# Optimization experiments

Measured on AMD Instinct MI355X. Metric: run time of the kernel, lower is better.

## Reference

```python
import jax, jax.numpy as jnp
import numpy as np

B, T, F_IN, F_OUT = 16, 2048, 128, 128
ALPHA = 0.2  # LeakyReLU negative slope
MASK_VAL = -1e9


def setup_inputs() -> dict:
    key = jax.random.key(0)
    kx, kw, ka, kadj = jax.random.split(key, 4)
    # xavier_uniform-ish scale for W and a (gain=1.414)
    w_bound = 1.414 * np.sqrt(6.0 / (F_IN + F_OUT))
    a_bound = 1.414 * np.sqrt(6.0 / (2 * F_OUT + 1))
    x = jax.random.normal(kx, (B, T, F_IN), jnp.float32)
    W = jax.random.uniform(kw, (F_IN, F_OUT), jnp.float32, -w_bound, w_bound)
    a = jax.random.uniform(ka, (2 * F_OUT, 1), jnp.float32, -a_bound, a_bound)
    adj = jax.random.randint(kadj, (B, T, T), 0, 2, jnp.int32)
    return {"x": x, "adj": adj, "W": W, "a": a}


def reference(x, adj, W, a):
    # h: [B,T,F_OUT]
    h = jnp.einsum('btf,fo->bto', x, W)
    # Additive GAT score decomposition: e[b,i,j] = leakyrelu(h_i . a1 + h_j . a2)
    # Mathematically identical to cat([h_i,h_j]) @ a, without the BxTxTx2F tensor.
    a1 = a[:F_OUT, 0]   # [F_OUT]
    a2 = a[F_OUT:, 0]   # [F_OUT]
    s1 = h @ a1         # [B,T]
    s2 = h @ a2         # [B,T]
    e = jax.nn.leaky_relu(s1[:, :, None] + s2[:, None, :], ALPHA)  # [B,T,T]
    e = jnp.where(adj == 0, MASK_VAL, e)
    att = jax.nn.softmax(e, axis=-1)  # [B,T,T]
    # dropout=0.0 / eval mode -> identity
    return att @ h  # [B,T,F_OUT]
```

## Files before the change

kernel.cpp:

```cpp
#include <hip/hip_runtime.h>

#define TT 2048
#define NB 16
#define FD 128
#define ALPHA 0.2f

typedef __attribute__((ext_vector_type(8))) short short8;
typedef __attribute__((ext_vector_type(4))) float f32x4;
typedef __attribute__((ext_vector_type(16))) float f32x16;

static __device__ __forceinline__ unsigned short f2bf(float f) {
    unsigned u = __float_as_uint(f);
    u += 0x7FFF + ((u >> 16) & 1);
    return (unsigned short)(u >> 16);
}
static __device__ __forceinline__ float bf2f(unsigned short s) {
    return __uint_as_float(((unsigned)s) << 16);
}

__global__ __launch_bounds__(256) void k_pack(const int* __restrict__ adj,
                                              unsigned char* __restrict__ bm)
{
    const int tid = threadIdx.x;
    const int w = tid >> 6, l = tid & 63;
    const int row = blockIdx.x * 4 + w;
    const int* ap = adj + (size_t)row * TT;
    unsigned char* op = bm + (size_t)row * 256;

    #pragma unroll
    for (int rd = 0; rd < 8; ++rd) {
        int4 q = *reinterpret_cast<const int4*>(ap + rd * 256 + l * 4);
        unsigned long long m0 = __ballot(q.x != 0);
        unsigned long long m1 = __ballot(q.y != 0);
        unsigned long long m2 = __ballot(q.z != 0);
        unsigned long long m3 = __ballot(q.w != 0);
        if (l < 32) {
            unsigned b =
                 ((unsigned)(m0 >> (2 * l)) & 1)
              | (((unsigned)(m1 >> (2 * l)) & 1) << 1)
              | (((unsigned)(m2 >> (2 * l)) & 1) << 2)
              | (((unsigned)(m3 >> (2 * l)) & 1) << 3)
              | (((unsigned)(m0 >> (2 * l + 1)) & 1) << 4)
              | (((unsigned)(m1 >> (2 * l + 1)) & 1) << 5)
              | (((unsigned)(m2 >> (2 * l + 1)) & 1) << 6)
              | (((unsigned)(m3 >> (2 * l + 1)) & 1) << 7);
            op[rd * 32 + l] = (unsigned char)b;
        }
    }
}

__global__ __launch_bounds__(256) void k_wt(const float* __restrict__ W,
                                            unsigned short* __restrict__ WT)
{
    int fid = blockIdx.x * 256 + threadIdx.x;
    int k = fid >> 5;
    int f = (fid & 31) << 2;
    float4 w4 = *reinterpret_cast<const float4*>(W + k * FD + f);
    WT[(f + 0) * FD + k] = f2bf(w4.x);
    WT[(f + 1) * FD + k] = f2bf(w4.y);
    WT[(f + 2) * FD + k] = f2bf(w4.z);
    WT[(f + 3) * FD + k] = f2bf(w4.w);
}

__global__ __launch_bounds__(256) void k_h(const float* __restrict__ x,
                                           const unsigned short* __restrict__ WT,
                                           const float* __restrict__ a,
                                           unsigned short* __restrict__ hF,
                                           float* __restrict__ s1,
                                           float* __restrict__ s2)
{
    __shared__ unsigned short hs[128][72];

    const int tid = threadIdx.x;
    const int b  = blockIdx.x >> 5;
    const int t0 = (blockIdx.x & 31) << 6;
    const int w = tid >> 6, l = tid & 63, g = l >> 4, r15 = l & 15;

    const float* xrow = x + ((size_t)(b * TT + t0 + w * 16 + r15)) * FD;

    f32x4 acc[8] = {};

    #pragma unroll
    for (int m = 0; m < 4; ++m) {
        const int koff = m * 32 + g * 8;
        float4 xa = *reinterpret_cast<const float4*>(xrow + koff);
        float4 xb = *reinterpret_cast<const float4*>(xrow + koff + 4);
        short8 af;
        af[0] = (short)f2bf(xa.x); af[1] = (short)f2bf(xa.y);
        af[2] = (short)f2bf(xa.z); af[3] = (short)f2bf(xa.w);
        af[4] = (short)f2bf(xb.x); af[5] = (short)f2bf(xb.y);
        af[6] = (short)f2bf(xb.z); af[7] = (short)f2bf(xb.w);
        #pragma unroll
        for (int n = 0; n < 8; ++n) {
            short8 bfr = *reinterpret_cast<const short8*>(WT + (n * 16 + r15) * FD + koff);
            acc[n] = __builtin_amdgcn_mfma_f32_16x16x32_bf16(af, bfr, acc[n], 0, 0, 0);
        }
    }

    float p1[4] = {0.f, 0.f, 0.f, 0.f}, p2[4] = {0.f, 0.f, 0.f, 0.f};
    #pragma unroll
    for (int n = 0; n < 8; ++n) {
        float a1v = a[n * 16 + r15];
        float a2v = a[FD + n * 16 + r15];
        #pragma unroll
        for (int r = 0; r < 4; ++r) {
            p1[r] += acc[n][r] * a1v;
            p2[r] += acc[n][r] * a2v;
        }
    }
    #pragma unroll
    for (int r = 0; r < 4; ++r) {
        #pragma unroll
        for (int off = 8; off >= 1; off >>= 1) {
            p1[r] += __shfl_xor(p1[r], off);
            p2[r] += __shfl_xor(p2[r], off);
        }
    }
    if (r15 == 0) {
        const int trow = t0 + w * 16 + g * 4;
        #pragma unroll
        for (int r = 0; r < 4; ++r) {
            s1[b * TT + trow + r] = p1[r];
            s2[b * TT + trow + r] = p2[r];
        }
    }

    #pragma unroll
    for (int n = 0; n < 8; ++n)
        #pragma unroll
        for (int r = 0; r < 4; ++r)
            hs[n * 16 + r15][w * 16 + g * 4 + r] = f2bf(acc[n][r]);
    __syncthreads();

    #pragma unroll
    for (int it = 0; it < 4; ++it) {
        int idx = it * 256 + tid;
        int lp = idx & 63;
        int frag = idx >> 6;
        int n32 = frag & 3, tl = frag >> 2;
        int fsrc = n32 * 32 + (lp & 31);
        int tsrc = tl * 16 + (lp >> 5) * 8;
        short8 v = *reinterpret_cast<const short8*>(&hs[fsrc][tsrc]);
        *reinterpret_cast<short8*>(
            hF + (((size_t)(b * 128 + (t0 >> 4) + tl)) * 4 + n32) * 512 + lp * 8) = v;
    }
}

__global__ __launch_bounds__(256, 4) void k_att(const unsigned char* __restrict__ bm,
                                                const unsigned short* __restrict__ hF,
                                                const float* __restrict__ s1,
                                                const float* __restrict__ s2,
                                                float* __restrict__ out)
{
    __shared__ __align__(16) float red[2][32][132];
    __shared__ float dsum[4][32];

    const int tid = threadIdx.x;
    const int wg = (blockIdx.x & 7) * 128 + (blockIdx.x >> 3);
    const int b  = wg >> 6;
    const int i0 = (wg & 63) << 5;
    const int w = tid >> 6, l = tid & 63;
    const int il = l & 31, h = l >> 5;
    const int hsh = h * 8;

    const int jbeg = w * (TT / 4);
    const float s1v = s1[b * TT + i0 + il];
    const float* s2p = s2 + b * TT + jbeg + h * 8;
    const unsigned char* bmrow = bm + ((size_t)(b * TT + i0 + il)) * 256 + w * 64;
    const unsigned short* hfp = hF + ((size_t)(b * 128 + (jbeg >> 4))) * 4 * 512 + l * 8;

    f32x16 acc[4] = {};
    float rsum = 0.f;

    short8 bb[2][4];
    #pragma unroll
    for (int n = 0; n < 4; ++n)
        bb[0][n] = *reinterpret_cast<const short8*>(hfp + (size_t)n * 512);

    uint4 bq;

    #pragma unroll
    for (int t = 0; t < 32; ++t) {
        const int cur = t & 1;
        if (t < 31) {
            #pragma unroll
            for (int n = 0; n < 4; ++n)
                bb[cur ^ 1][n] = *reinterpret_cast<const short8*>(
                    hfp + (size_t)((t + 1) * 4 + n) * 512);
        }
        if ((t & 7) == 0)
            bq = *reinterpret_cast<const uint4*>(bmrow + (t >> 3) * 16);
        const int wi = (t & 7) >> 1;
        const unsigned wsel = wi == 0 ? bq.x : wi == 1 ? bq.y : wi == 2 ? bq.z : bq.w;
        const unsigned bits = (wsel >> ((t & 1) * 16 + hsh)) & 0xffu;

        float4 sa = *reinterpret_cast<const float4*>(s2p + t * 16);
        float4 sb = *reinterpret_cast<const float4*>(s2p + t * 16 + 4);
        float csf[8] = {sa.x, sa.y, sa.z, sa.w, sb.x, sb.y, sb.z, sb.w};
        short8 af;
        #pragma unroll
        for (int e = 0; e < 8; ++e) {
            float s = s1v + csf[e];
            s = fmaxf(s, ALPHA * s);
            float p = ((bits >> e) & 1) ? __expf(s) : 0.f;
            unsigned short u = f2bf(p);
            rsum += bf2f(u);
            af[e] = (short)u;
        }
        #pragma unroll
        for (int n = 0; n < 4; ++n)
            acc[n] = __builtin_amdgcn_mfma_f32_32x32x16_bf16(af, bb[cur][n], acc[n], 0, 0, 0);
    }

    rsum += __shfl_xor(rsum, 32);
    if (l < 32) dsum[w][l] = rsum;

    if (w < 2) {
        #pragma unroll
        for (int n = 0; n < 4; ++n)
            #pragma unroll
            for (int r = 0; r < 16; ++r) {
                int irow = (r & 3) + 8 * (r >> 2) + 4 * h;
                red[w][irow][n * 32 + il] = acc[n][r];
            }
    }
    __syncthreads();
    if (w >= 2) {
        #pragma unroll
        for (int n = 0; n < 4; ++n)
            #pragma unroll
            for (int r = 0; r < 16; ++r) {
                int irow = (r & 3) + 8 * (r >> 2) + 4 * h;
                red[w - 2][irow][n * 32 + il] += acc[n][r];
            }
    }
    __syncthreads();

    #pragma unroll
    for (int it = 0; it < 4; ++it) {
        int e = it * 256 + tid;
        int row = e >> 5;
        int c4 = (e & 31) << 2;
        float4 v0 = *reinterpret_cast<const float4*>(&red[0][row][c4]);
        float4 v1 = *reinterpret_cast<const float4*>(&red[1][row][c4]);
        float dn = dsum[0][row] + dsum[1][row] + dsum[2][row] + dsum[3][row];
        float ri = 1.0f / dn;
        float4 o;
        o.x = (v0.x + v1.x) * ri;
        o.y = (v0.y + v1.y) * ri;
        o.z = (v0.z + v1.z) * ri;
        o.w = (v0.w + v1.w) * ri;
        *reinterpret_cast<float4*>(out + ((size_t)(b * TT + i0 + row)) * FD + c4) = o;
    }
}

extern "C" void kernel_launch(void* const* d_in, const int* in_sizes, int n_in,
                              void* d_out, int out_size, void* d_ws, size_t ws_size,
                              hipStream_t stream)
{
    const float* x  = (const float*)d_in[0];
    const int* adj  = (const int*)d_in[1];
    const float* W  = (const float*)d_in[2];
    const float* a  = (const float*)d_in[3];
    float* out = (float*)d_out;

    unsigned short* hF = (unsigned short*)d_ws;
    float* s1 = (float*)((char*)d_ws + (size_t)NB * FD * TT * 2);
    float* s2 = s1 + NB * TT;
    unsigned short* WT = (unsigned short*)(s2 + NB * TT);
    unsigned char* bm = (unsigned char*)(WT + FD * FD);

    k_pack<<<NB * TT / 4, 256, 0, stream>>>(adj, bm);
    k_wt  <<<16, 256, 0, stream>>>(W, WT);
    k_h   <<<NB * (TT / 64), 256, 0, stream>>>(x, WT, a, hF, s1, s2);
    k_att <<<NB * (TT / 32), 256, 0, stream>>>(bm, hF, s1, s2, out);
}
```

Baseline: 103.7 us.

## Merge adjacency packing, W transpose and h projection into one prep kernel

Replaces three prologue kernels with a single k_prep launch. The first 512 blocks each transpose and convert W into LDS themselves and compute h, s1 and s2. The remaining blocks pack the adjacency into a bitmask. This removes two kernel launches and their serialization, and lets the bandwidth-heavy adj packing overlap with the projection. In exchange, every projection block redundantly rebuilds the bf16 W^T in shared memory, and the larger LDS footprint may lower occupancy for the packing blocks.

After: 106.2 us. 2.5% more time.

```diff
diff --git a/kernel.cpp b/kernel.cpp
--- a/kernel.cpp
+++ b/kernel.cpp
@@ -18,63 +18,63 @@
     return __uint_as_float(((unsigned)s) << 16);
 }
 
-__global__ __launch_bounds__(256) void k_pack(const int* __restrict__ adj,
+__global__ __launch_bounds__(256) void k_prep(const float* __restrict__ x,
+                                              const float* __restrict__ W,
+                                              const float* __restrict__ a,
+                                              const int* __restrict__ adj,
+                                              unsigned short* __restrict__ hF,
+                                              float* __restrict__ s1,
+                                              float* __restrict__ s2,
                                               unsigned char* __restrict__ bm)
 {
+    __shared__ unsigned short lds[128 * 136];
+
     const int tid = threadIdx.x;
     const int w = tid >> 6, l = tid & 63;
-    const int row = blockIdx.x * 4 + w;
-    const int* ap = adj + (size_t)row * TT;
-    unsigned char* op = bm + (size_t)row * 256;
-
-    #pragma unroll
-    for (int rd = 0; rd < 8; ++rd) {
-        int4 q = *reinterpret_cast<const int4*>(ap + rd * 256 + l * 4);
-        unsigned long long m0 = __ballot(q.x != 0);
-        unsigned long long m1 = __ballot(q.y != 0);
-        unsigned long long m2 = __ballot(q.z != 0);
-        unsigned long long m3 = __ballot(q.w != 0);
-        if (l < 32) {
-            unsigned b =
-                 ((unsigned)(m0 >> (2 * l)) & 1)
-              | (((unsigned)(m1 >> (2 * l)) & 1) << 1)
-              | (((unsigned)(m2 >> (2 * l)) & 1) << 2)
-              | (((unsigned)(m3 >> (2 * l)) & 1) << 3)
-              | (((unsigned)(m0 >> (2 * l + 1)) & 1) << 4)
-              | (((unsigned)(m1 >> (2 * l + 1)) & 1) << 5)
-              | (((unsigned)(m2 >> (2 * l + 1)) & 1) << 6)
-              | (((unsigned)(m3 >> (2 * l + 1)) & 1) << 7);
-            op[rd * 32 + l] = (unsigned char)b;
-        }
-    }
-}
-
-__global__ __launch_bounds__(256) void k_wt(const float* __restrict__ W,
-                                            unsigned short* __restrict__ WT)
-{
-    int fid = blockIdx.x * 256 + threadIdx.x;
-    int k = fid >> 5;
-    int f = (fid & 31) << 2;
-    float4 w4 = *reinterpret_cast<const float4*>(W + k * FD + f);
-    WT[(f + 0) * FD + k] = f2bf(w4.x);
-    WT[(f + 1) * FD + k] = f2bf(w4.y);
-    WT[(f + 2) * FD + k] = f2bf(w4.z);
-    WT[(f + 3) * FD + k] = f2bf(w4.w);
-}
-
-__global__ __launch_bounds__(256) void k_h(const float* __restrict__ x,
-                                           const unsigned short* __restrict__ WT,
-                                           const float* __restrict__ a,
-                                           unsigned short* __restrict__ hF,
-                                           float* __restrict__ s1,
-                                           float* __restrict__ s2)
-{
-    __shared__ unsigned short hs[128][72];
-
-    const int tid = threadIdx.x;
+
+    if (blockIdx.x >= 512) {
+        const int row = (blockIdx.x - 512) * 4 + w;
+        const int* ap = adj + (size_t)row * TT;
+        unsigned char* op = bm + (size_t)row * 256;
+
+        #pragma unroll
+        for (int rd = 0; rd < 8; ++rd) {
+            int4 q = *reinterpret_cast<const int4*>(ap + rd * 256 + l * 4);
+            unsigned long long m0 = __ballot(q.x != 0);
+            unsigned long long m1 = __ballot(q.y != 0);
+            unsigned long long m2 = __ballot(q.z != 0);
+            unsigned long long m3 = __ballot(q.w != 0);
+            if (l < 32) {
+                unsigned b =
+                     ((unsigned)(m0 >> (2 * l)) & 1)
+                  | (((unsigned)(m1 >> (2 * l)) & 1) << 1)
+                  | (((unsigned)(m2 >> (2 * l)) & 1) << 2)
+                  | (((unsigned)(m3 >> (2 * l)) & 1) << 3)
+                  | (((unsigned)(m0 >> (2 * l + 1)) & 1) << 4)
+                  | (((unsigned)(m1 >> (2 * l + 1)) & 1) << 5)
+                  | (((unsigned)(m2 >> (2 * l + 1)) & 1) << 6)
+                  | (((unsigned)(m3 >> (2 * l + 1)) & 1) << 7);
+                op[rd * 32 + l] = (unsigned char)b;
+            }
+        }
+        return;
+    }
+
     const int b  = blockIdx.x >> 5;
     const int t0 = (blockIdx.x & 31) << 6;
-    const int w = tid >> 6, l = tid & 63, g = l >> 4, r15 = l & 15;
+    const int g = l >> 4, r15 = l & 15;
+
+    for (int it = 0; it < 16; ++it) {
+        int fid = it * 256 + tid;
+        int k = fid >> 5;
+        int f = (fid & 31) << 2;
+        float4 w4 = *reinterpret_cast<const float4*>(W + k * FD + f);
+        lds[(f + 0) * 136 + k] = f2bf(w4.x);
+        lds[(f + 1) * 136 + k] = f2bf(w4.y);
+        lds[(f + 2) * 136 + k] = f2bf(w4.z);
+        lds[(f + 3) * 136 + k] = f2bf(w4.w);
+    }
+    __syncthreads();
 
     const float* xrow = x + ((size_t)(b * TT + t0 + w * 16 + r15)) * FD;
 
@@ -92,7 +92,7 @@
         af[6] = (short)f2bf(xb.z); af[7] = (short)f2bf(xb.w);
         #pragma unroll
         for (int n = 0; n < 8; ++n) {
-            short8 bfr = *reinterpret_cast<const short8*>(WT + (n * 16 + r15) * FD + koff);
+            short8 bfr = *reinterpret_cast<const short8*>(&lds[(n * 16 + r15) * 136 + koff]);
             acc[n] = __builtin_amdgcn_mfma_f32_16x16x32_bf16(af, bfr, acc[n], 0, 0, 0);
         }
     }
@@ -125,11 +125,13 @@
         }
     }
 
+    __syncthreads();
+
     #pragma unroll
     for (int n = 0; n < 8; ++n)
         #pragma unroll
         for (int r = 0; r < 4; ++r)
-            hs[n * 16 + r15][w * 16 + g * 4 + r] = f2bf(acc[n][r]);
+            lds[(n * 16 + r15) * 72 + w * 16 + g * 4 + r] = f2bf(acc[n][r]);
     __syncthreads();
 
     #pragma unroll
@@ -140,7 +142,7 @@
         int n32 = frag & 3, tl = frag >> 2;
         int fsrc = n32 * 32 + (lp & 31);
         int tsrc = tl * 16 + (lp >> 5) * 8;
-        short8 v = *reinterpret_cast<const short8*>(&hs[fsrc][tsrc]);
+        short8 v = *reinterpret_cast<const short8*>(&lds[fsrc * 72 + tsrc]);
         *reinterpret_cast<short8*>(
             hF + (((size_t)(b * 128 + (t0 >> 4) + tl)) * 4 + n32) * 512 + lp * 8) = v;
     }
@@ -267,11 +269,8 @@
     unsigned short* hF = (unsigned short*)d_ws;
     float* s1 = (float*)((char*)d_ws + (size_t)NB * FD * TT * 2);
     float* s2 = s1 + NB * TT;
-    unsigned short* WT = (unsigned short*)(s2 + NB * TT);
-    unsigned char* bm = (unsigned char*)(WT + FD * FD);
-
-    k_pack<<<NB * TT / 4, 256, 0, stream>>>(adj, bm);
-    k_wt  <<<16, 256, 0, stream>>>(W, WT);
-    k_h   <<<NB * (TT / 64), 256, 0, stream>>>(x, WT, a, hF, s1, s2);
+    unsigned char* bm = (unsigned char*)(s2 + NB * TT);
+
+    k_prep<<<512 + NB * TT / 4, 256, 0, stream>>>(x, W, a, adj, hF, s1, s2, bm);
     k_att <<<NB * (TT / 32), 256, 0, stream>>>(bm, hF, s1, s2, out);
 }
```

## Merge adjacency packing into h projection kernel and use intrinsic bf16 conversion

Applied to the files above, without the earlier changes.

Folds the adjacency bit-packing kernel into the h/score projection kernel: the first 512 blocks compute h and the scores, and the remaining blocks pack the mask. This removes one launch and lets the two independent prep stages run at the same time. The attention inner loop now sums the row denominator from fp32 probabilities instead of the bf16-rounded values, tests mask bits with a shift and sign check, and converts to bf16 through the HIP intrinsic. The denominator now differs slightly from the bf16 numerator weights, and launch_bounds(256,8) may limit registers in the merged kernel.

Result: no change. 104.6 us (+0.9%).

```diff
diff --git a/kernel.cpp b/kernel.cpp
--- a/kernel.cpp
+++ b/kernel.cpp
@@ -1,4 +1,5 @@
 #include <hip/hip_runtime.h>
+#include <hip/hip_bf16.h>
 
 #define TT 2048
 #define NB 16
@@ -14,39 +15,8 @@
     u += 0x7FFF + ((u >> 16) & 1);
     return (unsigned short)(u >> 16);
 }
-static __device__ __forceinline__ float bf2f(unsigned short s) {
-    return __uint_as_float(((unsigned)s) << 16);
-}
-
-__global__ __launch_bounds__(256) void k_pack(const int* __restrict__ adj,
-                                              unsigned char* __restrict__ bm)
-{
-    const int tid = threadIdx.x;
-    const int w = tid >> 6, l = tid & 63;
-    const int row = blockIdx.x * 4 + w;
-    const int* ap = adj + (size_t)row * TT;
-    unsigned char* op = bm + (size_t)row * 256;
-
-    #pragma unroll
-    for (int rd = 0; rd < 8; ++rd) {
-        int4 q = *reinterpret_cast<const int4*>(ap + rd * 256 + l * 4);
-        unsigned long long m0 = __ballot(q.x != 0);
-        unsigned long long m1 = __ballot(q.y != 0);
-        unsigned long long m2 = __ballot(q.z != 0);
-        unsigned long long m3 = __ballot(q.w != 0);
-        if (l < 32) {
-            unsigned b =
-                 ((unsigned)(m0 >> (2 * l)) & 1)
-              | (((unsigned)(m1 >> (2 * l)) & 1) << 1)
-              | (((unsigned)(m2 >> (2 * l)) & 1) << 2)
-              | (((unsigned)(m3 >> (2 * l)) & 1) << 3)
-              | (((unsigned)(m0 >> (2 * l + 1)) & 1) << 4)
-              | (((unsigned)(m1 >> (2 * l + 1)) & 1) << 5)
-              | (((unsigned)(m2 >> (2 * l + 1)) & 1) << 6)
-              | (((unsigned)(m3 >> (2 * l + 1)) & 1) << 7);
-            op[rd * 32 + l] = (unsigned char)b;
-        }
-    }
+static __device__ __forceinline__ unsigned short bfbits(float f) {
+    return __builtin_bit_cast(unsigned short, __float2bfloat16(f));
 }
 
 __global__ __launch_bounds__(256) void k_wt(const float* __restrict__ W,
@@ -62,19 +32,51 @@
     WT[(f + 3) * FD + k] = f2bf(w4.w);
 }
 
-__global__ __launch_bounds__(256) void k_h(const float* __restrict__ x,
-                                           const unsigned short* __restrict__ WT,
-                                           const float* __restrict__ a,
-                                           unsigned short* __restrict__ hF,
-                                           float* __restrict__ s1,
-                                           float* __restrict__ s2)
+__global__ __launch_bounds__(256, 8) void k_prep(const float* __restrict__ x,
+                                                 const unsigned short* __restrict__ WT,
+                                                 const float* __restrict__ a,
+                                                 const int* __restrict__ adj,
+                                                 unsigned short* __restrict__ hF,
+                                                 float* __restrict__ s1,
+                                                 float* __restrict__ s2,
+                                                 unsigned char* __restrict__ bm)
 {
     __shared__ unsigned short hs[128][72];
 
     const int tid = threadIdx.x;
+    const int w = tid >> 6, l = tid & 63;
+
+    if (blockIdx.x >= 512) {
+        const int row = (blockIdx.x - 512) * 4 + w;
+        const int* ap = adj + (size_t)row * TT;
+        unsigned char* op = bm + (size_t)row * 256;
+
+        #pragma unroll
+        for (int rd = 0; rd < 8; ++rd) {
+            int4 q = *reinterpret_cast<const int4*>(ap + rd * 256 + l * 4);
+            unsigned long long m0 = __ballot(q.x != 0);
+            unsigned long long m1 = __ballot(q.y != 0);
+            unsigned long long m2 = __ballot(q.z != 0);
+            unsigned long long m3 = __ballot(q.w != 0);
+            if (l < 32) {
+                unsigned b =
+                     ((unsigned)(m0 >> (2 * l)) & 1)
+                  | (((unsigned)(m1 >> (2 * l)) & 1) << 1)
+                  | (((unsigned)(m2 >> (2 * l)) & 1) << 2)
+                  | (((unsigned)(m3 >> (2 * l)) & 1) << 3)
+                  | (((unsigned)(m0 >> (2 * l + 1)) & 1) << 4)
+                  | (((unsigned)(m1 >> (2 * l + 1)) & 1) << 5)
+                  | (((unsigned)(m2 >> (2 * l + 1)) & 1) << 6)
+                  | (((unsigned)(m3 >> (2 * l + 1)) & 1) << 7);
+                op[rd * 32 + l] = (unsigned char)b;
+            }
+        }
+        return;
+    }
+
     const int b  = blockIdx.x >> 5;
     const int t0 = (blockIdx.x & 31) << 6;
-    const int w = tid >> 6, l = tid & 63, g = l >> 4, r15 = l & 15;
+    const int g = l >> 4, r15 = l & 15;
 
     const float* xrow = x + ((size_t)(b * TT + t0 + w * 16 + r15)) * FD;
 
@@ -197,16 +199,19 @@
         float4 sa = *reinterpret_cast<const float4*>(s2p + t * 16);
         float4 sb = *reinterpret_cast<const float4*>(s2p + t * 16 + 4);
         float csf[8] = {sa.x, sa.y, sa.z, sa.w, sb.x, sb.y, sb.z, sb.w};
-        short8 af;
+        float pv[8];
         #pragma unroll
         for (int e = 0; e < 8; ++e) {
             float s = s1v + csf[e];
             s = fmaxf(s, ALPHA * s);
-            float p = ((bits >> e) & 1) ? __expf(s) : 0.f;
-            unsigned short u = f2bf(p);
-            rsum += bf2f(u);
-            af[e] = (short)u;
-        }
+            float p = ((int)(bits << (31 - e)) < 0) ? __expf(s) : 0.f;
+            rsum += p;
+            pv[e] = p;
+        }
+        short8 af;
+        #pragma unroll
+        for (int e = 0; e < 8; ++e)
+            af[e] = (short)bfbits(pv[e]);
         #pragma unroll
         for (int n = 0; n < 4; ++n)
             acc[n] = __builtin_amdgcn_mfma_f32_32x32x16_bf16(af, bb[cur][n], acc[n], 0, 0, 0);
@@ -270,8 +275,7 @@
     unsigned short* WT = (unsigned short*)(s2 + NB * TT);
     unsigned char* bm = (unsigned char*)(WT + FD * FD);
 
-    k_pack<<<NB * TT / 4, 256, 0, stream>>>(adj, bm);
     k_wt  <<<16, 256, 0, stream>>>(W, WT);
-    k_h   <<<NB * (TT / 64), 256, 0, stream>>>(x, WT, a, hF, s1, s2);
+    k_prep<<<512 + NB * TT / 4, 256, 0, stream>>>(x, WT, a, adj, hF, s1, s2, bm);
     k_att <<<NB * (TT / 32), 256, 0, stream>>>(bm, hF, s1, s2, out);
 }
```
